# Optimization experiments

Measured on AMD Instinct MI355X. Metric: run time of the kernel, lower is better.

Reference implementation:

```python
import jax, jax.numpy as jnp
import numpy as np

N = 100000
E = 1000000
D = 64


def setup_inputs() -> dict:
    key = jax.random.key(0)
    k1, k2, k3 = jax.random.split(key, 3)
    x = jax.random.normal(k1, (N, D), dtype=jnp.float32)
    edge_index = jax.random.randint(k2, (2, E), 0, N, dtype=jnp.int64)
    W = jax.random.normal(k3, (D, D), dtype=jnp.float32) * (1.0 / np.sqrt(D))  # nn.Linear weight [out, in]
    return {"x": x, "edge_index": edge_index, "W": W, "num_nodes": N}


def reference(x, edge_index, W, num_nodes):
    src, dst = edge_index[0], edge_index[1]
    # in-degree (counted on dst) + self loop
    deg = jnp.zeros((num_nodes,), dtype=x.dtype).at[dst].add(1.0) + 1.0
    dis = deg ** -0.5  # deg^{-1/2}, shape [N]
    # gather src features, scale by deg_inv_sqrt[src], scatter-add to dst
    msg = x[src] * dis[src][:, None]  # [E, D]
    agg = jnp.zeros_like(x).at[dst].add(msg)  # [N, D]
    # self-loop contribution, then scale by deg_inv_sqrt on the node axis
    agg = (agg + x * dis[:, None]) * dis[:, None]
    # linear (no bias): agg @ W^T with W of shape [out, in]
    return agg @ W.T
```

## Files before the change

kernel.cpp:

```cpp
#include <hip/hip_runtime.h>

#define FD 64

typedef __attribute__((ext_vector_type(8))) short bf16x8;
typedef __attribute__((ext_vector_type(4))) float f32x4;

__device__ inline short f2bf(float f) {
    union { float f; unsigned u; } v; v.f = f;
    unsigned r = (v.u + 0x7fffu + ((v.u >> 16) & 1u)) >> 16;
    return (short)r;
}

__global__ void degpos_kernel(const int* __restrict__ dst, int* __restrict__ degi,
                              int* __restrict__ pos, int E) {
    int i = blockIdx.x * blockDim.x + threadIdx.x;
    int stride = gridDim.x * blockDim.x;
    for (; i < E; i += stride) {
        pos[i] = atomicAdd(&degi[dst[i]], 1);
    }
}

#define SCAN_ELEMS 2048

__global__ void scan1_kernel(const int* __restrict__ degi, int* __restrict__ offs,
                             int* __restrict__ bsums, float* __restrict__ dis, int N) {
    __shared__ int tsum[256];
    int base = blockIdx.x * SCAN_ELEMS + threadIdx.x * 8;
    int v[8];
    int s = 0;
    #pragma unroll
    for (int k = 0; k < 8; ++k) {
        int idx = base + k;
        v[k] = (idx < N) ? degi[idx] : 0;
        if (idx < N) dis[idx] = rsqrtf((float)v[k] + 1.0f);
        s += v[k];
    }
    tsum[threadIdx.x] = s;
    __syncthreads();
    for (int off = 1; off < 256; off <<= 1) {
        int t = (threadIdx.x >= off) ? tsum[threadIdx.x - off] : 0;
        __syncthreads();
        tsum[threadIdx.x] += t;
        __syncthreads();
    }
    int excl = (threadIdx.x == 0) ? 0 : tsum[threadIdx.x - 1];
    #pragma unroll
    for (int k = 0; k < 8; ++k) {
        int idx = base + k;
        if (idx < N) offs[idx] = excl;
        excl += v[k];
    }
    if (threadIdx.x == 255) bsums[blockIdx.x] = tsum[255];
}

__global__ void scan2_kernel(int* __restrict__ bsums, int nb) {
    __shared__ int t[256];
    int v = (threadIdx.x < nb) ? bsums[threadIdx.x] : 0;
    t[threadIdx.x] = v;
    __syncthreads();
    for (int off = 1; off < 256; off <<= 1) {
        int u = (threadIdx.x >= off) ? t[threadIdx.x - off] : 0;
        __syncthreads();
        t[threadIdx.x] += u;
        __syncthreads();
    }
    if (threadIdx.x < nb) bsums[threadIdx.x] = (threadIdx.x == 0) ? 0 : t[threadIdx.x - 1];
}

__global__ void scan3_kernel(int* __restrict__ offs, const int* __restrict__ bsums, int N) {
    int i = blockIdx.x * blockDim.x + threadIdx.x;
    if (i < N) offs[i] += bsums[i / SCAN_ELEMS];
}

__global__ void fill_pos_kernel(const int* __restrict__ src, const int* __restrict__ dst,
                                const int* __restrict__ offs, const int* __restrict__ pos,
                                int* __restrict__ bucket, int E) {
    int i = blockIdx.x * blockDim.x + threadIdx.x;
    int stride = gridDim.x * blockDim.x;
    for (; i < E; i += stride) {
        bucket[offs[dst[i]] + pos[i]] = src[i];
    }
}

__global__ __launch_bounds__(256) void z_mfma_kernel(
        const float* __restrict__ x, const float* __restrict__ dis,
        const float* __restrict__ W, float* __restrict__ z, int N) {
    int lane = threadIdx.x & 63;
    int r16  = lane & 15;
    int kg   = lane >> 4;

    bf16x8 bfrag[4][2];
    #pragma unroll
    for (int ct = 0; ct < 4; ++ct) {
        #pragma unroll
        for (int kk = 0; kk < 2; ++kk) {
            const float* wp = W + (size_t)(ct * 16 + r16) * FD + kk * 32 + kg * 8;
            float4 w0 = *(const float4*)wp;
            float4 w1 = *(const float4*)(wp + 4);
            bf16x8 b;
            b[0] = f2bf(w0.x); b[1] = f2bf(w0.y); b[2] = f2bf(w0.z); b[3] = f2bf(w0.w);
            b[4] = f2bf(w1.x); b[5] = f2bf(w1.y); b[6] = f2bf(w1.z); b[7] = f2bf(w1.w);
            bfrag[ct][kk] = b;
        }
    }

    int wid    = blockIdx.x * (blockDim.x >> 6) + (threadIdx.x >> 6);
    int nwaves = gridDim.x * (blockDim.x >> 6);
    int tiles  = (N + 15) >> 4;

    for (int t = wid; t < tiles; t += nwaves) {
        int n0  = t << 4;
        int row = n0 + r16;
        int rl  = row < N ? row : N - 1;
        const float* xp = x + (size_t)rl * FD + kg * 8;
        float4 a00 = *(const float4*)(xp);
        float4 a01 = *(const float4*)(xp + 4);
        float4 a10 = *(const float4*)(xp + 32);
        float4 a11 = *(const float4*)(xp + 36);
        bf16x8 a0, a1;
        a0[0] = f2bf(a00.x); a0[1] = f2bf(a00.y); a0[2] = f2bf(a00.z); a0[3] = f2bf(a00.w);
        a0[4] = f2bf(a01.x); a0[5] = f2bf(a01.y); a0[6] = f2bf(a01.z); a0[7] = f2bf(a01.w);
        a1[0] = f2bf(a10.x); a1[1] = f2bf(a10.y); a1[2] = f2bf(a10.z); a1[3] = f2bf(a10.w);
        a1[4] = f2bf(a11.x); a1[5] = f2bf(a11.y); a1[6] = f2bf(a11.z); a1[7] = f2bf(a11.w);

        f32x4 acc[4];
        #pragma unroll
        for (int ct = 0; ct < 4; ++ct) {
            acc[ct] = (f32x4){0.f, 0.f, 0.f, 0.f};
            acc[ct] = __builtin_amdgcn_mfma_f32_16x16x32_bf16(a0, bfrag[ct][0], acc[ct], 0, 0, 0);
            acc[ct] = __builtin_amdgcn_mfma_f32_16x16x32_bf16(a1, bfrag[ct][1], acc[ct], 0, 0, 0);
        }

        #pragma unroll
        for (int reg = 0; reg < 4; ++reg) {
            int nr = n0 + kg * 4 + reg;
            if (nr < N) {
                float dn = dis[nr];
                #pragma unroll
                for (int ct = 0; ct < 4; ++ct) {
                    z[(size_t)nr * FD + ct * 16 + r16] = acc[ct][reg] * dn;
                }
            }
        }
    }
}

__global__ __launch_bounds__(256) void gather_z_kernel(
        const float* __restrict__ z, const int* __restrict__ offs,
        const int* __restrict__ degi, const int* __restrict__ bucket,
        const float* __restrict__ dis, float* __restrict__ out, int N) {
    int wave = threadIdx.x >> 6;
    int lane = threadIdx.x & 63;
    int n = blockIdx.x * 4 + wave;
    if (n >= N) return;

    int j   = offs[n];
    int end = j + degi[n];
    float acc = 0.0f;
    for (; j + 7 < end; j += 8) {
        int s0 = bucket[j],     s1 = bucket[j + 1], s2 = bucket[j + 2], s3 = bucket[j + 3];
        int s4 = bucket[j + 4], s5 = bucket[j + 5], s6 = bucket[j + 6], s7 = bucket[j + 7];
        float v0 = z[(size_t)s0 * FD + lane];
        float v1 = z[(size_t)s1 * FD + lane];
        float v2 = z[(size_t)s2 * FD + lane];
        float v3 = z[(size_t)s3 * FD + lane];
        float v4 = z[(size_t)s4 * FD + lane];
        float v5 = z[(size_t)s5 * FD + lane];
        float v6 = z[(size_t)s6 * FD + lane];
        float v7 = z[(size_t)s7 * FD + lane];
        acc += ((v0 + v1) + (v2 + v3)) + ((v4 + v5) + (v6 + v7));
    }
    for (; j + 3 < end; j += 4) {
        int s0 = bucket[j], s1 = bucket[j + 1], s2 = bucket[j + 2], s3 = bucket[j + 3];
        float v0 = z[(size_t)s0 * FD + lane];
        float v1 = z[(size_t)s1 * FD + lane];
        float v2 = z[(size_t)s2 * FD + lane];
        float v3 = z[(size_t)s3 * FD + lane];
        acc += (v0 + v1) + (v2 + v3);
    }
    for (; j < end; ++j) {
        acc += z[(size_t)bucket[j] * FD + lane];
    }
    out[(size_t)n * FD + lane] = (acc + z[(size_t)n * FD + lane]) * dis[n];
}

__global__ void deg_kernel(const int* __restrict__ dst, int* __restrict__ degi, int E) {
    int i = blockIdx.x * blockDim.x + threadIdx.x;
    int stride = gridDim.x * blockDim.x;
    for (; i < E; i += stride) {
        atomicAdd(&degi[dst[i]], 1);
    }
}

__global__ void fill_kernel(const int* __restrict__ src, const int* __restrict__ dst,
                            const int* __restrict__ offs, int* __restrict__ cursor,
                            int* __restrict__ bucket, int E) {
    int i = blockIdx.x * blockDim.x + threadIdx.x;
    int stride = gridDim.x * blockDim.x;
    for (; i < E; i += stride) {
        int d = dst[i];
        int p = atomicAdd(&cursor[d], 1);
        bucket[offs[d] + p] = src[i];
    }
}

__global__ __launch_bounds__(256) void gather_linear_kernel(
        const float* __restrict__ x, const int* __restrict__ offs,
        const int* __restrict__ degi, const int* __restrict__ bucket,
        const float* __restrict__ dis, const float* __restrict__ W,
        float* __restrict__ out, int N) {
    __shared__ float Wt[FD][FD + 1];
    __shared__ float rows[4][FD];

    for (int t = threadIdx.x; t < FD * FD; t += 256) {
        Wt[t & 63][t >> 6] = W[t];
    }
    __syncthreads();

    int wave = threadIdx.x >> 6;
    int lane = threadIdx.x & 63;
    int n = blockIdx.x * 4 + wave;

    if (n < N) {
        int j   = offs[n];
        int end = j + degi[n];
        float acc = 0.0f;
        for (; j + 3 < end; j += 4) {
            int s0 = bucket[j], s1 = bucket[j + 1], s2 = bucket[j + 2], s3 = bucket[j + 3];
            float d0 = dis[s0], d1 = dis[s1], d2 = dis[s2], d3 = dis[s3];
            float v0 = x[(size_t)s0 * FD + lane];
            float v1 = x[(size_t)s1 * FD + lane];
            float v2 = x[(size_t)s2 * FD + lane];
            float v3 = x[(size_t)s3 * FD + lane];
            acc += v0 * d0 + v1 * d1 + v2 * d2 + v3 * d3;
        }
        for (; j < end; ++j) {
            int s = bucket[j];
            acc += x[(size_t)s * FD + lane] * dis[s];
        }
        float dn = dis[n];
        rows[wave][lane] = (acc + x[(size_t)n * FD + lane] * dn) * dn;
    }
    if (n < N) {
        float o = 0.0f;
        #pragma unroll
        for (int i = 0; i < FD; i += 4) {
            float4 r = *(const float4*)&rows[wave][i];
            o += r.x * Wt[i + 0][lane]
               + r.y * Wt[i + 1][lane]
               + r.z * Wt[i + 2][lane]
               + r.w * Wt[i + 3][lane];
        }
        out[(size_t)n * FD + lane] = o;
    }
}

extern "C" void kernel_launch(void* const* d_in, const int* in_sizes, int n_in,
                              void* d_out, int out_size, void* d_ws, size_t ws_size,
                              hipStream_t stream) {
    const float* x  = (const float*)d_in[0];
    const int*   ei = (const int*)d_in[1];
    const float* W  = (const float*)d_in[2];

    const int N = in_sizes[0] / FD;
    const int E = in_sizes[1] / 2;
    const int* src = ei;
    const int* dst = ei + E;

    float* out = (float*)d_out;
    const int nb = (N + SCAN_ELEMS - 1) / SCAN_ELEMS;

    size_t need_full = ((size_t)N * 3 + 1024 + (size_t)E * 2 + (size_t)N * FD) * 4;

    if (ws_size >= need_full) {
        char* ws = (char*)d_ws;
        int*   degi   = (int*)ws;    ws += (size_t)N * 4;
        float* dis    = (float*)ws;  ws += (size_t)N * 4;
        int*   offs   = (int*)ws;    ws += (size_t)N * 4;
        int*   bsums  = (int*)ws;    ws += 1024 * 4;
        int*   pos    = (int*)ws;    ws += (size_t)E * 4;
        int*   bucket = (int*)ws;    ws += (size_t)E * 4;
        float* z      = (float*)ws;

        hipMemsetAsync(degi, 0, (size_t)N * 4, stream);
        degpos_kernel<<<2048, 256, 0, stream>>>(dst, degi, pos, E);
        scan1_kernel<<<nb, 256, 0, stream>>>(degi, offs, bsums, dis, N);
        scan2_kernel<<<1, 256, 0, stream>>>(bsums, nb);
        scan3_kernel<<<(N + 255) / 256, 256, 0, stream>>>(offs, bsums, N);
        z_mfma_kernel<<<512, 256, 0, stream>>>(x, dis, W, z, N);
        fill_pos_kernel<<<2048, 256, 0, stream>>>(src, dst, offs, pos, bucket, E);
        gather_z_kernel<<<(N + 3) / 4, 256, 0, stream>>>(z, offs, degi, bucket, dis, out, N);
    } else {
        char* ws = (char*)d_ws;
        int*   degi   = (int*)ws;    ws += (size_t)N * 4;
        float* dis    = (float*)ws;  ws += (size_t)N * 4;
        int*   offs   = (int*)ws;    ws += (size_t)N * 4;
        int*   cursor = (int*)ws;    ws += (size_t)N * 4;
        int*   bsums  = (int*)ws;    ws += 1024 * 4;
        int*   bucket = (int*)ws;

        hipMemsetAsync(degi,   0, (size_t)N * 4, stream);
        hipMemsetAsync(cursor, 0, (size_t)N * 4, stream);
        deg_kernel<<<2048, 256, 0, stream>>>(dst, degi, E);
        scan1_kernel<<<nb, 256, 0, stream>>>(degi, offs, bsums, dis, N);
        scan2_kernel<<<1, 256, 0, stream>>>(bsums, nb);
        scan3_kernel<<<(N + 255) / 256, 256, 0, stream>>>(offs, bsums, N);
        fill_kernel<<<2048, 256, 0, stream>>>(src, dst, offs, cursor, bucket, E);
        gather_linear_kernel<<<(N + 3) / 4, 256, 0, stream>>>(
            x, offs, degi, bucket, dis, W, out, N);
    }
}
```

Measured before the change: 141.2 us.

## Store z in bf16, pack pos as uint16, drop scan3 pass

The intermediate z = x·Wᵀ·dis is now stored as bf16, which halves the bytes moved by the random per-edge gathers. The per-edge slot index is stored as 16-bit, which halves that buffer's traffic. The scan3 kernel is removed, and the block-level scan offsets are added inline in the fill and gather kernels. The costs are extra bf16 rounding error in the aggregation, and the assumption that in-degree fits in 16 bits.

```diff
diff --git a/kernel.cpp b/kernel.cpp
--- a/kernel.cpp
+++ b/kernel.cpp
@@ -10,13 +10,17 @@
     unsigned r = (v.u + 0x7fffu + ((v.u >> 16) & 1u)) >> 16;
     return (short)r;
 }
+__device__ inline float bf2f(unsigned short u) {
+    union { unsigned u; float f; } v; v.u = ((unsigned)u) << 16;
+    return v.f;
+}
 
 __global__ void degpos_kernel(const int* __restrict__ dst, int* __restrict__ degi,
-                              int* __restrict__ pos, int E) {
+                              unsigned short* __restrict__ pos, int E) {
     int i = blockIdx.x * blockDim.x + threadIdx.x;
     int stride = gridDim.x * blockDim.x;
     for (; i < E; i += stride) {
-        pos[i] = atomicAdd(&degi[dst[i]], 1);
+        pos[i] = (unsigned short)atomicAdd(&degi[dst[i]], 1);
     }
 }
 
@@ -73,18 +77,20 @@
 }
 
 __global__ void fill_pos_kernel(const int* __restrict__ src, const int* __restrict__ dst,
-                                const int* __restrict__ offs, const int* __restrict__ pos,
+                                const int* __restrict__ offs, const int* __restrict__ bsums,
+                                const unsigned short* __restrict__ pos,
                                 int* __restrict__ bucket, int E) {
     int i = blockIdx.x * blockDim.x + threadIdx.x;
     int stride = gridDim.x * blockDim.x;
     for (; i < E; i += stride) {
-        bucket[offs[dst[i]] + pos[i]] = src[i];
+        int d = dst[i];
+        bucket[offs[d] + bsums[d >> 11] + (int)pos[i]] = src[i];
     }
 }
 
 __global__ __launch_bounds__(256) void z_mfma_kernel(
         const float* __restrict__ x, const float* __restrict__ dis,
-        const float* __restrict__ W, float* __restrict__ z, int N) {
+        const float* __restrict__ W, unsigned short* __restrict__ z, int N) {
     int lane = threadIdx.x & 63;
     int r16  = lane & 15;
     int kg   = lane >> 4;
@@ -138,7 +144,8 @@
                 float dn = dis[nr];
                 #pragma unroll
                 for (int ct = 0; ct < 4; ++ct) {
-                    z[(size_t)nr * FD + ct * 16 + r16] = acc[ct][reg] * dn;
+                    z[(size_t)nr * FD + ct * 16 + r16] =
+                        (unsigned short)f2bf(acc[ct][reg] * dn);
                 }
             }
         }
@@ -146,42 +153,44 @@
 }
 
 __global__ __launch_bounds__(256) void gather_z_kernel(
-        const float* __restrict__ z, const int* __restrict__ offs,
-        const int* __restrict__ degi, const int* __restrict__ bucket,
-        const float* __restrict__ dis, float* __restrict__ out, int N) {
+        const unsigned short* __restrict__ z, const int* __restrict__ offs,
+        const int* __restrict__ bsums, const int* __restrict__ degi,
+        const int* __restrict__ bucket, const float* __restrict__ dis,
+        float* __restrict__ out, int N) {
     int wave = threadIdx.x >> 6;
     int lane = threadIdx.x & 63;
     int n = blockIdx.x * 4 + wave;
     if (n >= N) return;
 
-    int j   = offs[n];
+    const unsigned short* zl = z + lane;
+    int j   = offs[n] + bsums[n >> 11];
     int end = j + degi[n];
     float acc = 0.0f;
     for (; j + 7 < end; j += 8) {
         int s0 = bucket[j],     s1 = bucket[j + 1], s2 = bucket[j + 2], s3 = bucket[j + 3];
         int s4 = bucket[j + 4], s5 = bucket[j + 5], s6 = bucket[j + 6], s7 = bucket[j + 7];
-        float v0 = z[(size_t)s0 * FD + lane];
-        float v1 = z[(size_t)s1 * FD + lane];
-        float v2 = z[(size_t)s2 * FD + lane];
-        float v3 = z[(size_t)s3 * FD + lane];
-        float v4 = z[(size_t)s4 * FD + lane];
-        float v5 = z[(size_t)s5 * FD + lane];
-        float v6 = z[(size_t)s6 * FD + lane];
-        float v7 = z[(size_t)s7 * FD + lane];
+        float v0 = bf2f(zl[(size_t)s0 * FD]);
+        float v1 = bf2f(zl[(size_t)s1 * FD]);
+        float v2 = bf2f(zl[(size_t)s2 * FD]);
+        float v3 = bf2f(zl[(size_t)s3 * FD]);
+        float v4 = bf2f(zl[(size_t)s4 * FD]);
+        float v5 = bf2f(zl[(size_t)s5 * FD]);
+        float v6 = bf2f(zl[(size_t)s6 * FD]);
+        float v7 = bf2f(zl[(size_t)s7 * FD]);
         acc += ((v0 + v1) + (v2 + v3)) + ((v4 + v5) + (v6 + v7));
     }
     for (; j + 3 < end; j += 4) {
         int s0 = bucket[j], s1 = bucket[j + 1], s2 = bucket[j + 2], s3 = bucket[j + 3];
-        float v0 = z[(size_t)s0 * FD + lane];
-        float v1 = z[(size_t)s1 * FD + lane];
-        float v2 = z[(size_t)s2 * FD + lane];
-        float v3 = z[(size_t)s3 * FD + lane];
+        float v0 = bf2f(zl[(size_t)s0 * FD]);
+        float v1 = bf2f(zl[(size_t)s1 * FD]);
+        float v2 = bf2f(zl[(size_t)s2 * FD]);
+        float v3 = bf2f(zl[(size_t)s3 * FD]);
         acc += (v0 + v1) + (v2 + v3);
     }
     for (; j < end; ++j) {
-        acc += z[(size_t)bucket[j] * FD + lane];
-    }
-    out[(size_t)n * FD + lane] = (acc + z[(size_t)n * FD + lane]) * dis[n];
+        acc += bf2f(zl[(size_t)bucket[j] * FD]);
+    }
+    out[(size_t)n * FD + lane] = (acc + bf2f(zl[(size_t)n * FD])) * dis[n];
 }
 
 __global__ void deg_kernel(const int* __restrict__ dst, int* __restrict__ degi, int E) {
@@ -270,7 +279,8 @@
     float* out = (float*)d_out;
     const int nb = (N + SCAN_ELEMS - 1) / SCAN_ELEMS;
 
-    size_t need_full = ((size_t)N * 3 + 1024 + (size_t)E * 2 + (size_t)N * FD) * 4;
+    size_t posB = (((size_t)E * 2) + 3) & ~(size_t)3;
+    size_t need_full = ((size_t)N * 3 + 1024 + (size_t)E) * 4 + posB + (size_t)N * FD * 2;
 
     if (ws_size >= need_full) {
         char* ws = (char*)d_ws;
@@ -278,18 +288,17 @@
         float* dis    = (float*)ws;  ws += (size_t)N * 4;
         int*   offs   = (int*)ws;    ws += (size_t)N * 4;
         int*   bsums  = (int*)ws;    ws += 1024 * 4;
-        int*   pos    = (int*)ws;    ws += (size_t)E * 4;
         int*   bucket = (int*)ws;    ws += (size_t)E * 4;
-        float* z      = (float*)ws;
+        unsigned short* pos = (unsigned short*)ws;  ws += posB;
+        unsigned short* z   = (unsigned short*)ws;
 
         hipMemsetAsync(degi, 0, (size_t)N * 4, stream);
         degpos_kernel<<<2048, 256, 0, stream>>>(dst, degi, pos, E);
         scan1_kernel<<<nb, 256, 0, stream>>>(degi, offs, bsums, dis, N);
         scan2_kernel<<<1, 256, 0, stream>>>(bsums, nb);
-        scan3_kernel<<<(N + 255) / 256, 256, 0, stream>>>(offs, bsums, N);
         z_mfma_kernel<<<512, 256, 0, stream>>>(x, dis, W, z, N);
-        fill_pos_kernel<<<2048, 256, 0, stream>>>(src, dst, offs, pos, bucket, E);
-        gather_z_kernel<<<(N + 3) / 4, 256, 0, stream>>>(z, offs, degi, bucket, dis, out, N);
+        fill_pos_kernel<<<2048, 256, 0, stream>>>(src, dst, offs, bsums, pos, bucket, E);
+        gather_z_kernel<<<(N + 3) / 4, 256, 0, stream>>>(z, offs, bsums, degi, bucket, dis, out, N);
     } else {
         char* ws = (char*)d_ws;
         int*   degi   = (int*)ws;    ws += (size_t)N * 4;
```

Result: faster. 134.8 us (-4.5%).
